# Optimization experiments

Measured on AMD Instinct MI355X. Metric: run time of the kernel, lower is better.

Reference implementation:

```python
import jax, jax.numpy as jnp
import numpy as np

E = 1024  # dim_model
H = 16    # num_heads
HD = E // H
B, S = 32, 2048
LN_EPS = 1e-5


def setup_inputs() -> dict:
    key = jax.random.key(0)
    ks = jax.random.split(key, 8)
    x = jax.random.normal(ks[0], (B, S, E), dtype=jnp.float32)
    key_padding_mask = jax.random.randint(ks[1], (B, S), 0, 2).astype(jnp.int32)
    # learned seed (xavier_uniform over [1,1,E])
    bound = float(np.sqrt(6.0 / (1 + E)))
    seed = jax.random.uniform(ks[2], (1, 1, E), minval=-bound, maxval=bound, dtype=jnp.float32)
    # MHA params: packed in_proj [3E, E] (q,k,v stacked) + bias, out_proj [E,E]+bias
    w_scale = 1.0 / np.sqrt(E)
    in_proj_w = jax.random.uniform(ks[3], (3 * E, E), minval=-w_scale, maxval=w_scale, dtype=jnp.float32)
    in_proj_b = jnp.zeros((3 * E,), dtype=jnp.float32)
    out_w = jax.random.uniform(ks[4], (E, E), minval=-w_scale, maxval=w_scale, dtype=jnp.float32)
    out_b = jnp.zeros((E,), dtype=jnp.float32)
    ln_g = jnp.ones((E,), dtype=jnp.float32)
    ln_b = jnp.zeros((E,), dtype=jnp.float32)
    return {"x": x, "key_padding_mask": key_padding_mask, "seed": seed,
            "in_proj_w": in_proj_w, "in_proj_b": in_proj_b,
            "out_w": out_w, "out_b": out_b, "ln_g": ln_g, "ln_b": ln_b}


def reference(x, key_padding_mask, seed, in_proj_w, in_proj_b, out_w, out_b, ln_g, ln_b):
    wq, wk, wv = in_proj_w[:E], in_proj_w[E:2 * E], in_proj_w[2 * E:]
    bq, bk, bv = in_proj_b[:E], in_proj_b[E:2 * E], in_proj_b[2 * E:]
    # q from single learned seed: [1,1,E] -> [1,H,1,HD] (broadcast over batch)
    q = (seed @ wq.T + bq).reshape(1, 1, H, HD).transpose(0, 2, 1, 3)
    k = (x @ wk.T + bk).reshape(x.shape[0], -1, H, HD).transpose(0, 2, 1, 3)  # [B,H,S,HD]
    v = (x @ wv.T + bv).reshape(x.shape[0], -1, H, HD).transpose(0, 2, 1, 3)
    scale = 1.0 / jnp.sqrt(jnp.asarray(HD, dtype=x.dtype))
    scores = jnp.einsum('bhqd,bhkd->bhqk', q * scale, k)  # broadcasts q batch dim -> [B,H,1,S]
    pad = (key_padding_mask == 0)[:, None, None, :]  # True = pad
    scores = jnp.where(pad, -jnp.inf, scores)
    attn = jax.nn.softmax(scores, axis=-1)
    ctx = jnp.einsum('bhqk,bhkd->bhqd', attn, v)  # [B,H,1,HD]
    ctx = ctx.transpose(0, 2, 1, 3).reshape(x.shape[0], E)  # squeeze single query
    out = ctx @ out_w.T + out_b
    mu = jnp.mean(out, axis=-1, keepdims=True)
    var = jnp.mean(jnp.square(out - mu), axis=-1, keepdims=True)
    return (out - mu) / jnp.sqrt(var + LN_EPS) * ln_g + ln_b
```

## Files before the change

### kernel.cpp

```cpp
#include <hip/hip_runtime.h>
#include <hip/hip_bf16.h>
#include <math.h>

#define E 1024
#define H 16
#define HD 64
#define B 32
#define S 2048
#define CH 16
#define CTOK (S / CH)
#define SUB 32
#define NSUB (CTOK / SUB)
#define BHE (B * H * E)

typedef __attribute__((ext_vector_type(8))) short short8;
typedef __attribute__((ext_vector_type(4))) float f32x4;

__device__ __forceinline__ short f2bf(float f) {
    union { __hip_bfloat16 h; short s; } u;
    u.h = __float2bfloat16(f);
    return u.s;
}

__global__ __launch_bounds__(256) void qproj_kernel(const float* __restrict__ W,
                                                    const float* __restrict__ bqkv,
                                                    const float* __restrict__ seed,
                                                    float* __restrict__ q) {
    int gw = (blockIdx.x * 256 + threadIdx.x) >> 6;
    int lane = threadIdx.x & 63;
    if (gw >= E) return;
    const float4* row = (const float4*)(W + (size_t)gw * E);
    const float4* sd = (const float4*)seed;
    float acc = 0.f;
#pragma unroll
    for (int k = 0; k < 4; ++k) {
        float4 w4 = row[k * 64 + lane];
        float4 s4 = sd[k * 64 + lane];
        acc = fmaf(w4.x, s4.x, acc); acc = fmaf(w4.y, s4.y, acc);
        acc = fmaf(w4.z, s4.z, acc); acc = fmaf(w4.w, s4.w, acc);
    }
#pragma unroll
    for (int off = 32; off > 0; off >>= 1) acc += __shfl_down(acc, off, 64);
    if (lane == 0) q[gw] = acc + bqkv[gw];
}

__global__ __launch_bounds__(256) void uproj_kernel(const float* __restrict__ W,
                                                    const float* __restrict__ q,
                                                    short* __restrict__ ubf) {
    int h = blockIdx.y;
    int e = blockIdx.x * 256 + threadIdx.x;
    __shared__ float qs[HD];
    if (threadIdx.x < HD) qs[threadIdx.x] = q[h * HD + threadIdx.x];
    __syncthreads();
    const float* Wk = W + ((size_t)(E + h * HD)) * E + e;
    float acc = 0.f;
#pragma unroll 8
    for (int d = 0; d < HD; ++d) acc = fmaf(qs[d], Wk[(size_t)d * E], acc);
    ubf[(size_t)h * E + e] = f2bf(acc * 0.125f);
}

__global__ __launch_bounds__(512, 4) void fused_kernel(const float* __restrict__ x,
                                                       const int* __restrict__ mask,
                                                       const short* __restrict__ ubf,
                                                       float* __restrict__ part,
                                                       float* __restrict__ mstat,
                                                       float* __restrict__ lstat) {
    int ss = blockIdx.x, b = blockIdx.y;
    __shared__ short xB[SUB * E];
    __shared__ float scp[8 * 64 * 4];
    __shared__ float pcur[SUB * H];
    __shared__ int   mk[CTOK];
    __shared__ float mrun[H], lrun[H], rfac[H];
    __shared__ float wred[8][16];

    int tid = threadIdx.x, lane = tid & 63, wid = tid >> 6;

    if (tid < H) { mrun[tid] = -1e30f; lrun[tid] = 0.f; }
    for (int i = tid; i < CTOK; i += 512) mk[i] = mask[(size_t)b * S + ss * CTOK + i];

    float2 a2[16];
#pragma unroll
    for (int h = 0; h < 16; ++h) a2[h] = make_float2(0.f, 0.f);

    __syncthreads();

    for (int sub = 0; sub < NSUB; ++sub) {
        int t0 = sub * SUB;

        {
            int tok = tid >> 4;
            int es  = tid & 15;
            const float* xr = x + ((size_t)b * S + ss * CTOK + t0 + tok) * E;
            bool live = mk[t0 + tok] != 0;
#pragma unroll
            for (int i = 0; i < 8; ++i) {
                int e0 = (es + i * 16) * 8;
                if (live) {
                    float4 lo = *(const float4*)(xr + e0);
                    float4 hi = *(const float4*)(xr + e0 + 4);
                    short8 v;
                    v[0] = f2bf(lo.x); v[1] = f2bf(lo.y); v[2] = f2bf(lo.z); v[3] = f2bf(lo.w);
                    v[4] = f2bf(hi.x); v[5] = f2bf(hi.y); v[6] = f2bf(hi.z); v[7] = f2bf(hi.w);
                    int byte = (tok * 2048 + e0 * 2) ^ ((tok & 7) << 4);
                    *(short8*)((char*)xB + byte) = v;
                }
            }
        }
        __syncthreads();

        {
            int tw = wid & 1, kq = wid >> 1;
            int tr = lane & 15, kg = lane >> 4;
            int tok = tw * 16 + tr;
            f32x4 acc = {0.f, 0.f, 0.f, 0.f};
            const short* ub = ubf + (size_t)tr * E;
#pragma unroll
            for (int st = 0; st < 8; ++st) {
                int e0 = kq * 256 + st * 32 + kg * 8;
                int byte = (tok * 2048 + e0 * 2) ^ ((tok & 7) << 4);
                short8 a = *(const short8*)((char*)xB + byte);
                short8 bv = *(const short8*)(ub + e0);
                acc = __builtin_amdgcn_mfma_f32_16x16x32_bf16(a, bv, acc, 0, 0, 0);
            }
            *(f32x4*)&scp[(wid * 64 + lane) * 4] = acc;
        }
        __syncthreads();

        {
            int tok = tid >> 4, h = tid & 15;
            int tw = tok >> 4, r = tok & 3, kg2 = (tok & 15) >> 2;
            float s = 0.f;
#pragma unroll
            for (int kq = 0; kq < 4; ++kq)
                s += scp[((kq * 2 + tw) * 64 + kg2 * 16 + h) * 4 + r];
            bool live = mk[t0 + tok] != 0;
            float sv = live ? s : -1e30f;
            float mx = sv;
            mx = fmaxf(mx, __shfl_xor(mx, 16, 64));
            mx = fmaxf(mx, __shfl_xor(mx, 32, 64));
            if (lane < 16) wred[wid][lane] = mx;
            __syncthreads();
            if (tid < 16) {
                float mt = wred[0][tid];
#pragma unroll
                for (int w = 1; w < 8; ++w) mt = fmaxf(mt, wred[w][tid]);
                float mo = mrun[tid];
                float mn = fmaxf(mo, mt);
                rfac[tid] = __expf(mo - mn);
                mrun[tid] = mn;
            }
            __syncthreads();
            float p = live ? __expf(s - mrun[h]) : 0.f;
            pcur[tok * 16 + h] = p;
            float ps = p;
            ps += __shfl_xor(ps, 16, 64);
            ps += __shfl_xor(ps, 32, 64);
            if (lane < 16) wred[wid][lane] = ps;
            __syncthreads();
            if (tid < 16) {
                float lt = 0.f;
#pragma unroll
                for (int w = 0; w < 8; ++w) lt += wred[w][tid];
                lrun[tid] = lrun[tid] * rfac[tid] + lt;
            }
        }
        __syncthreads();

        {
#pragma unroll
            for (int h = 0; h < 16; ++h) {
                float r = rfac[h];
                a2[h].x *= r; a2[h].y *= r;
            }
            int ebyte = tid * 4;
            for (int tok = 0; tok < SUB; ++tok) {
                if (!mk[t0 + tok]) continue;
                int byte = (tok * 2048 + ebyte) ^ ((tok & 7) << 4);
                unsigned xv2 = *(const unsigned*)((char*)xB + byte);
                float xe0 = __uint_as_float(xv2 << 16);
                float xe1 = __uint_as_float(xv2 & 0xffff0000u);
                const float4* pr = (const float4*)&pcur[tok * 16];
                float4 p0 = pr[0], p1 = pr[1], p2 = pr[2], p3 = pr[3];
                a2[0].x = fmaf(p0.x, xe0, a2[0].x);   a2[0].y = fmaf(p0.x, xe1, a2[0].y);
                a2[1].x = fmaf(p0.y, xe0, a2[1].x);   a2[1].y = fmaf(p0.y, xe1, a2[1].y);
                a2[2].x = fmaf(p0.z, xe0, a2[2].x);   a2[2].y = fmaf(p0.z, xe1, a2[2].y);
                a2[3].x = fmaf(p0.w, xe0, a2[3].x);   a2[3].y = fmaf(p0.w, xe1, a2[3].y);
                a2[4].x = fmaf(p1.x, xe0, a2[4].x);   a2[4].y = fmaf(p1.x, xe1, a2[4].y);
                a2[5].x = fmaf(p1.y, xe0, a2[5].x);   a2[5].y = fmaf(p1.y, xe1, a2[5].y);
                a2[6].x = fmaf(p1.z, xe0, a2[6].x);   a2[6].y = fmaf(p1.z, xe1, a2[6].y);
                a2[7].x = fmaf(p1.w, xe0, a2[7].x);   a2[7].y = fmaf(p1.w, xe1, a2[7].y);
                a2[8].x = fmaf(p2.x, xe0, a2[8].x);   a2[8].y = fmaf(p2.x, xe1, a2[8].y);
                a2[9].x = fmaf(p2.y, xe0, a2[9].x);   a2[9].y = fmaf(p2.y, xe1, a2[9].y);
                a2[10].x = fmaf(p2.z, xe0, a2[10].x); a2[10].y = fmaf(p2.z, xe1, a2[10].y);
                a2[11].x = fmaf(p2.w, xe0, a2[11].x); a2[11].y = fmaf(p2.w, xe1, a2[11].y);
                a2[12].x = fmaf(p3.x, xe0, a2[12].x); a2[12].y = fmaf(p3.x, xe1, a2[12].y);
                a2[13].x = fmaf(p3.y, xe0, a2[13].x); a2[13].y = fmaf(p3.y, xe1, a2[13].y);
                a2[14].x = fmaf(p3.z, xe0, a2[14].x); a2[14].y = fmaf(p3.z, xe1, a2[14].y);
                a2[15].x = fmaf(p3.w, xe0, a2[15].x); a2[15].y = fmaf(p3.w, xe1, a2[15].y);
            }
        }
        __syncthreads();
    }

    float* pb = part + ((size_t)ss * B + b) * (H * E) + tid * 2;
#pragma unroll
    for (int h = 0; h < 16; ++h) *(float2*)(pb + (size_t)h * E) = a2[h];
    if (tid < 16) {
        mstat[((size_t)ss * B + b) * H + tid] = mrun[tid];
        lstat[((size_t)ss * B + b) * H + tid] = lrun[tid];
    }
}

__global__ __launch_bounds__(256) void ctxc_kernel(const float* __restrict__ W,
                                                   const float* __restrict__ bqkv,
                                                   const float* __restrict__ part,
                                                   const float* __restrict__ mstat,
                                                   const float* __restrict__ lstat,
                                                   float* __restrict__ ctx) {
    int cb = blockIdx.x, b = blockIdx.y, t = threadIdx.x;
    int h0 = cb * 4;
    __shared__ float xls[4 * E];
    __shared__ float fs[4][CH];
    __shared__ float linv[4];
    if (t < 4) {
        int h = h0 + t;
        float mv[CH];
        float mg = -1e30f;
#pragma unroll
        for (int c = 0; c < CH; ++c) {
            mv[c] = mstat[((size_t)c * B + b) * H + h];
            mg = fmaxf(mg, mv[c]);
        }
        float l = 0.f;
#pragma unroll
        for (int c = 0; c < CH; ++c) {
            float fc = __expf(mv[c] - mg);
            fs[t][c] = fc;
            l = fmaf(fc, lstat[((size_t)c * B + b) * H + h], l);
        }
        linv[t] = 1.f / l;
    }
    __syncthreads();
    for (int i = t; i < 4 * E / 4; i += 256) {
        int hl = i >> 8, e4 = i & 255;
        float4 s = make_float4(0.f, 0.f, 0.f, 0.f);
#pragma unroll 4
        for (int c = 0; c < CH; ++c) {
            float fc = fs[hl][c];
            float4 v = ((const float4*)part)[(((size_t)c * B + b) * H + h0 + hl) * (E / 4) + e4];
            s.x = fmaf(fc, v.x, s.x); s.y = fmaf(fc, v.y, s.y);
            s.z = fmaf(fc, v.z, s.z); s.w = fmaf(fc, v.w, s.w);
        }
        float li = linv[hl];
        s.x *= li; s.y *= li; s.z *= li; s.w *= li;
        ((float4*)xls)[i] = s;
    }
    __syncthreads();
    int c = cb * 256 + t;
    int h = c >> 6;
    const float4* wr = (const float4*)(W + ((size_t)(2 * E + c)) * E);
    const float4* xl = (const float4*)(xls + (h - h0) * E);
    float acc = bqkv[2 * E + c];
#pragma unroll 4
    for (int e4 = 0; e4 < E / 4; ++e4) {
        float4 w = wr[e4], xv = xl[e4];
        acc = fmaf(w.x, xv.x, acc); acc = fmaf(w.y, xv.y, acc);
        acc = fmaf(w.z, xv.z, acc); acc = fmaf(w.w, xv.w, acc);
    }
    ctx[(size_t)b * E + c] = acc;
}

__global__ __launch_bounds__(256) void outproj_kernel(const float* __restrict__ Wo,
                                                      const float* __restrict__ ob,
                                                      const float* __restrict__ ctx,
                                                      float* __restrict__ outpre) {
    int obk = blockIdx.x, b = blockIdx.y, t = threadIdx.x;
    int o = obk * 256 + t;
    __shared__ float cl[E];
    const float4* cp = (const float4*)(ctx + (size_t)b * E);
    for (int i = t; i < E / 4; i += 256) ((float4*)cl)[i] = cp[i];
    __syncthreads();
    const float4* wr = (const float4*)(Wo + (size_t)o * E);
    const float4* cl4 = (const float4*)cl;
    float acc = ob[o];
#pragma unroll 4
    for (int e4 = 0; e4 < E / 4; ++e4) {
        float4 w = wr[e4], cv = cl4[e4];
        acc = fmaf(w.x, cv.x, acc); acc = fmaf(w.y, cv.y, acc);
        acc = fmaf(w.z, cv.z, acc); acc = fmaf(w.w, cv.w, acc);
    }
    outpre[(size_t)b * E + o] = acc;
}

__global__ __launch_bounds__(256) void ln_kernel(const float* __restrict__ outpre,
                                                 const float* __restrict__ g,
                                                 const float* __restrict__ bb,
                                                 float* __restrict__ out) {
    int b = blockIdx.x, t = threadIdx.x, lane = t & 63, wid = t >> 6;
    const float4* row = (const float4*)(outpre + (size_t)b * E);
    float4 v = row[t];
    float s = v.x + v.y + v.z + v.w;
    float sq = v.x * v.x + v.y * v.y + v.z * v.z + v.w * v.w;
    __shared__ float rs[4], rq[4];
#pragma unroll
    for (int off = 32; off > 0; off >>= 1) {
        s += __shfl_down(s, off, 64);
        sq += __shfl_down(sq, off, 64);
    }
    if (lane == 0) { rs[wid] = s; rq[wid] = sq; }
    __syncthreads();
    s = rs[0] + rs[1] + rs[2] + rs[3];
    sq = rq[0] + rq[1] + rq[2] + rq[3];
    float mean = s * (1.f / E);
    float var = sq * (1.f / E) - mean * mean;
    float inv = rsqrtf(var + 1e-5f);
    float4 gv = ((const float4*)g)[t];
    float4 bv = ((const float4*)bb)[t];
    float4 o;
    o.x = (v.x - mean) * inv * gv.x + bv.x;
    o.y = (v.y - mean) * inv * gv.y + bv.y;
    o.z = (v.z - mean) * inv * gv.z + bv.z;
    o.w = (v.w - mean) * inv * gv.w + bv.w;
    ((float4*)(out + (size_t)b * E))[t] = o;
}

extern "C" void kernel_launch(void* const* d_in, const int* in_sizes, int n_in,
                              void* d_out, int out_size, void* d_ws, size_t ws_size,
                              hipStream_t stream) {
    const float* x    = (const float*)d_in[0];
    const int*   mask = (const int*)d_in[1];
    const float* seed = (const float*)d_in[2];
    const float* W    = (const float*)d_in[3];
    const float* bqkv = (const float*)d_in[4];
    const float* Wo   = (const float*)d_in[5];
    const float* ob   = (const float*)d_in[6];
    const float* g    = (const float*)d_in[7];
    const float* lb   = (const float*)d_in[8];
    float* out = (float*)d_out;

    float* ws = (float*)d_ws;
    float* q      = ws;
    float* part   = q + E;
    float* mstat  = part + (size_t)CH * BHE;
    float* lstat  = mstat + (size_t)CH * B * H;
    short* ubf    = (short*)(lstat + (size_t)CH * B * H);
    float* ctx    = (float*)(ubf + (size_t)H * E);
    float* outpre = ctx + (size_t)B * E;

    qproj_kernel<<<256, 256, 0, stream>>>(W, bqkv, seed, q);
    uproj_kernel<<<dim3(E / 256, H), 256, 0, stream>>>(W, q, ubf);
    fused_kernel<<<dim3(CH, B), 512, 0, stream>>>(x, mask, ubf, part, mstat, lstat);
    ctxc_kernel<<<dim3(E / 256, B), 256, 0, stream>>>(W, bqkv, part, mstat, lstat, ctx);
    outproj_kernel<<<dim3(E / 256, B), 256, 0, stream>>>(Wo, ob, ctx, outpre);
    ln_kernel<<<B, 256, 0, stream>>>(outpre, g, lb, out);
}
```

Before: 131.3 us.

## Use MFMA for P·X accumulation and fuse q/u and outproj/LN kernels

```diff
diff --git a/kernel.cpp b/kernel.cpp
--- a/kernel.cpp
+++ b/kernel.cpp
@@ -12,6 +12,7 @@
 #define SUB 32
 #define NSUB (CTOK / SUB)
 #define BHE (B * H * E)
+#define PSTR 17
 
 typedef __attribute__((ext_vector_type(8))) short short8;
 typedef __attribute__((ext_vector_type(4))) float f32x4;
@@ -22,41 +23,38 @@
     return u.s;
 }
 
-__global__ __launch_bounds__(256) void qproj_kernel(const float* __restrict__ W,
-                                                    const float* __restrict__ bqkv,
-                                                    const float* __restrict__ seed,
-                                                    float* __restrict__ q) {
-    int gw = (blockIdx.x * 256 + threadIdx.x) >> 6;
-    int lane = threadIdx.x & 63;
-    if (gw >= E) return;
-    const float4* row = (const float4*)(W + (size_t)gw * E);
+__global__ __launch_bounds__(256) void qu_kernel(const float* __restrict__ W,
+                                                 const float* __restrict__ bqkv,
+                                                 const float* __restrict__ seed,
+                                                 short* __restrict__ ubf) {
+    int h = blockIdx.x, tid = threadIdx.x, lane = tid & 63, wv = tid >> 6;
+    __shared__ float qs[HD];
     const float4* sd = (const float4*)seed;
-    float acc = 0.f;
-#pragma unroll
-    for (int k = 0; k < 4; ++k) {
-        float4 w4 = row[k * 64 + lane];
-        float4 s4 = sd[k * 64 + lane];
-        acc = fmaf(w4.x, s4.x, acc); acc = fmaf(w4.y, s4.y, acc);
-        acc = fmaf(w4.z, s4.z, acc); acc = fmaf(w4.w, s4.w, acc);
-    }
-#pragma unroll
-    for (int off = 32; off > 0; off >>= 1) acc += __shfl_down(acc, off, 64);
-    if (lane == 0) q[gw] = acc + bqkv[gw];
-}
-
-__global__ __launch_bounds__(256) void uproj_kernel(const float* __restrict__ W,
-                                                    const float* __restrict__ q,
-                                                    short* __restrict__ ubf) {
-    int h = blockIdx.y;
-    int e = blockIdx.x * 256 + threadIdx.x;
-    __shared__ float qs[HD];
-    if (threadIdx.x < HD) qs[threadIdx.x] = q[h * HD + threadIdx.x];
-    __syncthreads();
-    const float* Wk = W + ((size_t)(E + h * HD)) * E + e;
-    float acc = 0.f;
+    for (int rr = 0; rr < 16; ++rr) {
+        int r = wv * 16 + rr;
+        const float4* row = (const float4*)(W + (size_t)(h * HD + r) * E);
+        float acc = 0.f;
+#pragma unroll
+        for (int k = 0; k < 4; ++k) {
+            float4 w4 = row[k * 64 + lane];
+            float4 s4 = sd[k * 64 + lane];
+            acc = fmaf(w4.x, s4.x, acc); acc = fmaf(w4.y, s4.y, acc);
+            acc = fmaf(w4.z, s4.z, acc); acc = fmaf(w4.w, s4.w, acc);
+        }
+#pragma unroll
+        for (int off = 32; off > 0; off >>= 1) acc += __shfl_down(acc, off, 64);
+        if (lane == 0) qs[r] = acc + bqkv[h * HD + r];
+    }
+    __syncthreads();
+#pragma unroll
+    for (int j = 0; j < 4; ++j) {
+        int e = tid + j * 256;
+        const float* Wk = W + ((size_t)(E + h * HD)) * E + e;
+        float acc = 0.f;
 #pragma unroll 8
-    for (int d = 0; d < HD; ++d) acc = fmaf(qs[d], Wk[(size_t)d * E], acc);
-    ubf[(size_t)h * E + e] = f2bf(acc * 0.125f);
+        for (int d = 0; d < HD; ++d) acc = fmaf(qs[d], Wk[(size_t)d * E], acc);
+        ubf[(size_t)h * E + e] = f2bf(acc * 0.125f);
+    }
 }
 
 __global__ __launch_bounds__(512, 4) void fused_kernel(const float* __restrict__ x,
@@ -68,19 +66,20 @@
     int ss = blockIdx.x, b = blockIdx.y;
     __shared__ short xB[SUB * E];
     __shared__ float scp[8 * 64 * 4];
-    __shared__ float pcur[SUB * H];
+    __shared__ float pcur[SUB * PSTR];
     __shared__ int   mk[CTOK];
     __shared__ float mrun[H], lrun[H], rfac[H];
     __shared__ float wred[8][16];
 
     int tid = threadIdx.x, lane = tid & 63, wid = tid >> 6;
+    int col = lane & 15, kg4 = lane >> 4;
 
     if (tid < H) { mrun[tid] = -1e30f; lrun[tid] = 0.f; }
     for (int i = tid; i < CTOK; i += 512) mk[i] = mask[(size_t)b * S + ss * CTOK + i];
 
-    float2 a2[16];
-#pragma unroll
-    for (int h = 0; h < 16; ++h) a2[h] = make_float2(0.f, 0.f);
+    f32x4 pacc[8];
+#pragma unroll
+    for (int et = 0; et < 8; ++et) pacc[et] = (f32x4){0.f, 0.f, 0.f, 0.f};
 
     __syncthreads();
 
@@ -92,32 +91,33 @@
             int es  = tid & 15;
             const float* xr = x + ((size_t)b * S + ss * CTOK + t0 + tok) * E;
             bool live = mk[t0 + tok] != 0;
+            int sw = (tok & 7) << 4;
 #pragma unroll
             for (int i = 0; i < 8; ++i) {
                 int e0 = (es + i * 16) * 8;
+                short8 v = (short8){0, 0, 0, 0, 0, 0, 0, 0};
                 if (live) {
                     float4 lo = *(const float4*)(xr + e0);
                     float4 hi = *(const float4*)(xr + e0 + 4);
-                    short8 v;
                     v[0] = f2bf(lo.x); v[1] = f2bf(lo.y); v[2] = f2bf(lo.z); v[3] = f2bf(lo.w);
                     v[4] = f2bf(hi.x); v[5] = f2bf(hi.y); v[6] = f2bf(hi.z); v[7] = f2bf(hi.w);
-                    int byte = (tok * 2048 + e0 * 2) ^ ((tok & 7) << 4);
-                    *(short8*)((char*)xB + byte) = v;
                 }
+                int byte = (tok * 2048 + e0 * 2) ^ sw;
+                *(short8*)((char*)xB + byte) = v;
             }
         }
         __syncthreads();
 
         {
             int tw = wid & 1, kq = wid >> 1;
-            int tr = lane & 15, kg = lane >> 4;
-            int tok = tw * 16 + tr;
-            f32x4 acc = {0.f, 0.f, 0.f, 0.f};
-            const short* ub = ubf + (size_t)tr * E;
+            int tok = tw * 16 + col;
+            int sw = (tok & 7) << 4;
+            f32x4 acc = (f32x4){0.f, 0.f, 0.f, 0.f};
+            const short* ub = ubf + (size_t)col * E;
 #pragma unroll
             for (int st = 0; st < 8; ++st) {
-                int e0 = kq * 256 + st * 32 + kg * 8;
-                int byte = (tok * 2048 + e0 * 2) ^ ((tok & 7) << 4);
+                int e0 = kq * 256 + st * 32 + kg4 * 8;
+                int byte = (tok * 2048 + e0 * 2) ^ sw;
                 short8 a = *(const short8*)((char*)xB + byte);
                 short8 bv = *(const short8*)(ub + e0);
                 acc = __builtin_amdgcn_mfma_f32_16x16x32_bf16(a, bv, acc, 0, 0, 0);
@@ -151,7 +151,7 @@
             }
             __syncthreads();
             float p = live ? __expf(s - mrun[h]) : 0.f;
-            pcur[tok * 16 + h] = p;
+            pcur[tok * PSTR + h] = p;
             float ps = p;
             ps += __shfl_xor(ps, 16, 64);
             ps += __shfl_xor(ps, 32, 64);
@@ -167,44 +167,42 @@
         __syncthreads();
 
         {
-#pragma unroll
-            for (int h = 0; h < 16; ++h) {
-                float r = rfac[h];
-                a2[h].x *= r; a2[h].y *= r;
-            }
-            int ebyte = tid * 4;
-            for (int tok = 0; tok < SUB; ++tok) {
-                if (!mk[t0 + tok]) continue;
-                int byte = (tok * 2048 + ebyte) ^ ((tok & 7) << 4);
-                unsigned xv2 = *(const unsigned*)((char*)xB + byte);
-                float xe0 = __uint_as_float(xv2 << 16);
-                float xe1 = __uint_as_float(xv2 & 0xffff0000u);
-                const float4* pr = (const float4*)&pcur[tok * 16];
-                float4 p0 = pr[0], p1 = pr[1], p2 = pr[2], p3 = pr[3];
-                a2[0].x = fmaf(p0.x, xe0, a2[0].x);   a2[0].y = fmaf(p0.x, xe1, a2[0].y);
-                a2[1].x = fmaf(p0.y, xe0, a2[1].x);   a2[1].y = fmaf(p0.y, xe1, a2[1].y);
-                a2[2].x = fmaf(p0.z, xe0, a2[2].x);   a2[2].y = fmaf(p0.z, xe1, a2[2].y);
-                a2[3].x = fmaf(p0.w, xe0, a2[3].x);   a2[3].y = fmaf(p0.w, xe1, a2[3].y);
-                a2[4].x = fmaf(p1.x, xe0, a2[4].x);   a2[4].y = fmaf(p1.x, xe1, a2[4].y);
-                a2[5].x = fmaf(p1.y, xe0, a2[5].x);   a2[5].y = fmaf(p1.y, xe1, a2[5].y);
-                a2[6].x = fmaf(p1.z, xe0, a2[6].x);   a2[6].y = fmaf(p1.z, xe1, a2[6].y);
-                a2[7].x = fmaf(p1.w, xe0, a2[7].x);   a2[7].y = fmaf(p1.w, xe1, a2[7].y);
-                a2[8].x = fmaf(p2.x, xe0, a2[8].x);   a2[8].y = fmaf(p2.x, xe1, a2[8].y);
-                a2[9].x = fmaf(p2.y, xe0, a2[9].x);   a2[9].y = fmaf(p2.y, xe1, a2[9].y);
-                a2[10].x = fmaf(p2.z, xe0, a2[10].x); a2[10].y = fmaf(p2.z, xe1, a2[10].y);
-                a2[11].x = fmaf(p2.w, xe0, a2[11].x); a2[11].y = fmaf(p2.w, xe1, a2[11].y);
-                a2[12].x = fmaf(p3.x, xe0, a2[12].x); a2[12].y = fmaf(p3.x, xe1, a2[12].y);
-                a2[13].x = fmaf(p3.y, xe0, a2[13].x); a2[13].y = fmaf(p3.y, xe1, a2[13].y);
-                a2[14].x = fmaf(p3.z, xe0, a2[14].x); a2[14].y = fmaf(p3.z, xe1, a2[14].y);
-                a2[15].x = fmaf(p3.w, xe0, a2[15].x); a2[15].y = fmaf(p3.w, xe1, a2[15].y);
+            float rf0 = rfac[kg4 * 4 + 0];
+            float rf1 = rfac[kg4 * 4 + 1];
+            float rf2 = rfac[kg4 * 4 + 2];
+            float rf3 = rfac[kg4 * 4 + 3];
+#pragma unroll
+            for (int et = 0; et < 8; ++et) {
+                pacc[et][0] *= rf0; pacc[et][1] *= rf1;
+                pacc[et][2] *= rf2; pacc[et][3] *= rf3;
+            }
+            short8 af;
+#pragma unroll
+            for (int j = 0; j < 8; ++j)
+                af[j] = f2bf(pcur[(kg4 * 8 + j) * PSTR + col]);
+            int ebase = wid * 128;
+#pragma unroll
+            for (int et = 0; et < 8; ++et) {
+                short8 bf;
+#pragma unroll
+                for (int j = 0; j < 8; ++j) {
+                    int tok = kg4 * 8 + j;
+                    int byte = (tok * 2048 + (ebase + et * 16 + col) * 2) ^ (j << 4);
+                    bf[j] = *(const short*)((const char*)xB + byte);
+                }
+                pacc[et] = __builtin_amdgcn_mfma_f32_16x16x32_bf16(af, bf, pacc[et], 0, 0, 0);
             }
         }
         __syncthreads();
     }
 
-    float* pb = part + ((size_t)ss * B + b) * (H * E) + tid * 2;
-#pragma unroll
-    for (int h = 0; h < 16; ++h) *(float2*)(pb + (size_t)h * E) = a2[h];
+    float* pb = part + ((size_t)ss * B + b) * (H * E);
+#pragma unroll
+    for (int et = 0; et < 8; ++et) {
+#pragma unroll
+        for (int r = 0; r < 4; ++r)
+            pb[(size_t)(kg4 * 4 + r) * E + wid * 128 + et * 16 + col] = pacc[et][r];
+    }
     if (tid < 16) {
         mstat[((size_t)ss * B + b) * H + tid] = mrun[tid];
         lstat[((size_t)ss * B + b) * H + tid] = lrun[tid];
@@ -270,58 +268,53 @@
     ctx[(size_t)b * E + c] = acc;
 }
 
-__global__ __launch_bounds__(256) void outproj_kernel(const float* __restrict__ Wo,
-                                                      const float* __restrict__ ob,
-                                                      const float* __restrict__ ctx,
-                                                      float* __restrict__ outpre) {
-    int obk = blockIdx.x, b = blockIdx.y, t = threadIdx.x;
-    int o = obk * 256 + t;
+__global__ __launch_bounds__(512) void outln_kernel(const float* __restrict__ Wo,
+                                                    const float* __restrict__ ob,
+                                                    const float* __restrict__ ctx,
+                                                    const float* __restrict__ g,
+                                                    const float* __restrict__ lb,
+                                                    float* __restrict__ out) {
+    int b = blockIdx.x, t = threadIdx.x, lane = t & 63, wv = t >> 6;
     __shared__ float cl[E];
+    __shared__ float rs[8], rq[8];
     const float4* cp = (const float4*)(ctx + (size_t)b * E);
-    for (int i = t; i < E / 4; i += 256) ((float4*)cl)[i] = cp[i];
-    __syncthreads();
-    const float4* wr = (const float4*)(Wo + (size_t)o * E);
-    const float4* cl4 = (const float4*)cl;
-    float acc = ob[o];
+    for (int i = t; i < E / 4; i += 512) ((float4*)cl)[i] = cp[i];
+    __syncthreads();
+    float acc[2];
+#pragma unroll
+    for (int j = 0; j < 2; ++j) {
+        int o = t + j * 512;
+        const float4* wr = (const float4*)(Wo + (size_t)o * E);
+        const float4* cl4 = (const float4*)cl;
+        float a = ob[o];
 #pragma unroll 4
-    for (int e4 = 0; e4 < E / 4; ++e4) {
-        float4 w = wr[e4], cv = cl4[e4];
-        acc = fmaf(w.x, cv.x, acc); acc = fmaf(w.y, cv.y, acc);
-        acc = fmaf(w.z, cv.z, acc); acc = fmaf(w.w, cv.w, acc);
-    }
-    outpre[(size_t)b * E + o] = acc;
-}
-
-__global__ __launch_bounds__(256) void ln_kernel(const float* __restrict__ outpre,
-                                                 const float* __restrict__ g,
-                                                 const float* __restrict__ bb,
-                                                 float* __restrict__ out) {
-    int b = blockIdx.x, t = threadIdx.x, lane = t & 63, wid = t >> 6;
-    const float4* row = (const float4*)(outpre + (size_t)b * E);
-    float4 v = row[t];
-    float s = v.x + v.y + v.z + v.w;
-    float sq = v.x * v.x + v.y * v.y + v.z * v.z + v.w * v.w;
-    __shared__ float rs[4], rq[4];
+        for (int e4 = 0; e4 < E / 4; ++e4) {
+            float4 w = wr[e4], cv = cl4[e4];
+            a = fmaf(w.x, cv.x, a); a = fmaf(w.y, cv.y, a);
+            a = fmaf(w.z, cv.z, a); a = fmaf(w.w, cv.w, a);
+        }
+        acc[j] = a;
+    }
+    float s = acc[0] + acc[1];
+    float sq = acc[0] * acc[0] + acc[1] * acc[1];
 #pragma unroll
     for (int off = 32; off > 0; off >>= 1) {
         s += __shfl_down(s, off, 64);
         sq += __shfl_down(sq, off, 64);
     }
-    if (lane == 0) { rs[wid] = s; rq[wid] = sq; }
-    __syncthreads();
-    s = rs[0] + rs[1] + rs[2] + rs[3];
-    sq = rq[0] + rq[1] + rq[2] + rq[3];
+    if (lane == 0) { rs[wv] = s; rq[wv] = sq; }
+    __syncthreads();
+    s = 0.f; sq = 0.f;
+#pragma unroll
+    for (int w = 0; w < 8; ++w) { s += rs[w]; sq += rq[w]; }
     float mean = s * (1.f / E);
     float var = sq * (1.f / E) - mean * mean;
     float inv = rsqrtf(var + 1e-5f);
-    float4 gv = ((const float4*)g)[t];
-    float4 bv = ((const float4*)bb)[t];
-    float4 o;
-    o.x = (v.x - mean) * inv * gv.x + bv.x;
-    o.y = (v.y - mean) * inv * gv.y + bv.y;
-    o.z = (v.z - mean) * inv * gv.z + bv.z;
-    o.w = (v.w - mean) * inv * gv.w + bv.w;
-    ((float4*)(out + (size_t)b * E))[t] = o;
+#pragma unroll
+    for (int j = 0; j < 2; ++j) {
+        int o = t + j * 512;
+        out[(size_t)b * E + o] = (acc[j] - mean) * inv * g[o] + lb[o];
+    }
 }
 
 extern "C" void kernel_launch(void* const* d_in, const int* in_sizes, int n_in,
@@ -339,18 +332,14 @@
     float* out = (float*)d_out;
 
     float* ws = (float*)d_ws;
-    float* q      = ws;
-    float* part   = q + E;
+    float* part   = ws;
     float* mstat  = part + (size_t)CH * BHE;
     float* lstat  = mstat + (size_t)CH * B * H;
     short* ubf    = (short*)(lstat + (size_t)CH * B * H);
     float* ctx    = (float*)(ubf + (size_t)H * E);
-    float* outpre = ctx + (size_t)B * E;
-
-    qproj_kernel<<<256, 256, 0, stream>>>(W, bqkv, seed, q);
-    uproj_kernel<<<dim3(E / 256, H), 256, 0, stream>>>(W, q, ubf);
+
+    qu_kernel<<<H, 256, 0, stream>>>(W, bqkv, seed, ubf);
     fused_kernel<<<dim3(CH, B), 512, 0, stream>>>(x, mask, ubf, part, mstat, lstat);
     ctxc_kernel<<<dim3(E / 256, B), 256, 0, stream>>>(W, bqkv, part, mstat, lstat, ctx);
-    outproj_kernel<<<dim3(E / 256, B), 256, 0, stream>>>(Wo, ob, ctx, outpre);
-    ln_kernel<<<B, 256, 0, stream>>>(outpre, g, lb, out);
-}
+    outln_kernel<<<B, 512, 0, stream>>>(Wo, ob, ctx, g, lb, out);
+}
```

Measured after the change: 221.7 us. 68.9% more time.
